# Optimization experiments

Hardware: AMD Instinct MI355X
Metric: run time of the kernel (lower is better)

Reference implementation:

```python
import jax, jax.numpy as jnp
import numpy as np
from jax import lax

BN_EPS = 1e-5


def _conv1d(h, w, b=None):
    # h: [B, Cin, L], w: [Cout, Cin, K], 'same' padding for odd K
    k = w.shape[-1]
    out = lax.conv_general_dilated(h, w, (1,), [(k // 2, k // 2)],
                                   dimension_numbers=('NCH', 'OIH', 'NCH'))
    if b is not None:
        out = out + b[None, :, None]
    return out


def _bn(h, gamma, beta):
    # eval-mode BatchNorm1d with running_mean=0, running_var=1
    return h * (gamma[None, :, None] / jnp.sqrt(1.0 + BN_EPS)) + beta[None, :, None]


def _encoder(h, cw, cb, rw, gammas, betas, aw, au):
    # h: [B, D, L] -> V: [B, C, F]
    t = jnp.tanh(_conv1d(h, cw, cb))
    t = _bn(t, gammas[0], betas[0])
    for i in range(rw.shape[0]):  # residual blocks
        t = jnp.tanh(_bn(_conv1d(t, rw[i]), gammas[i + 1], betas[i + 1]) + t)
    # label attention: w [A,F], u [C,A]
    Z = jnp.tanh(jnp.einsum('af,bfl->bal', aw, t))
    A = jax.nn.softmax(jnp.einsum('ca,bal->bcl', au, Z), axis=2)
    V = jnp.einsum('bfl,bcl->bcf', t, A)
    return V


def setup_inputs() -> dict:
    key = jax.random.key(0)
    ks = list(jax.random.split(key, 32))
    B, L, D, C, VOC, NE, N, E = 16, 4096, 256, 50, 50000, 20050, 512, 8192
    F, A, FFN = 100, 256, 128

    def rn(k, shape, s):
        return (jax.random.normal(k, shape, jnp.float32) * s).astype(jnp.float32)

    x = jax.random.randint(ks[0], (B, L), 0, VOC)
    attention_mask = jnp.ones((B, L), jnp.int32)
    nodes = jax.random.randint(ks[1], (B, N), 0, NE)
    src = jax.random.randint(ks[2], (B, E), 0, N)
    off = jax.random.randint(ks[3], (B, E), 1, N)
    dst = (src + off) % N  # guaranteed no self-loops
    edges = jnp.stack([src, dst], axis=1)  # [B, 2, E]

    inp = dict(x=x, attention_mask=attention_mask, nodes=nodes, edges=edges)
    inp['word_emb'] = rn(ks[4], (VOC, D), 0.02)
    inp['entity_emb'] = rn(ks[5], (NE, D), 0.02)
    i = 6
    for ksz in (3, 5, 9):
        inp[f'convw{ksz}'] = rn(ks[i], (F, D, ksz), (2.0 / (D * ksz)) ** 0.5); i += 1
        inp[f'convb{ksz}'] = jnp.zeros((F,), jnp.float32)
        inp[f'resw{ksz}'] = rn(ks[i], (2, F, F, ksz), (2.0 / (F * ksz)) ** 0.5); i += 1
    inp['bn_gamma'] = jnp.ones((3, 3, F), jnp.float32)
    inp['bn_beta'] = jnp.zeros((3, 3, F), jnp.float32)
    inp['attn_w'] = rn(ks[i], (3, A, F), 0.05); i += 1
    inp['attn_u'] = rn(ks[i], (3, C, A), 0.05); i += 1
    inp['gc1_w'] = rn(ks[i], (D, D), (1.0 / D) ** 0.5); i += 1
    inp['gc1_b'] = jnp.zeros((D,), jnp.float32)
    inp['gc2_w'] = rn(ks[i], (D, D), (1.0 / D) ** 0.5); i += 1
    inp['gc2_b'] = jnp.zeros((D,), jnp.float32)
    inp['fin1_w'] = rn(ks[i], (FFN, 3 * F + D), 0.05); i += 1
    inp['fin1_b'] = jnp.zeros((FFN,), jnp.float32)
    inp['fin2_w'] = rn(ks[i], (C, FFN), 0.05); i += 1
    inp['fin2_b'] = jnp.zeros((C,), jnp.float32)
    return inp


def reference(x, attention_mask, nodes, edges, word_emb, entity_emb,
              convw3, convb3, resw3, convw5, convb5, resw5, convw9, convb9, resw9,
              bn_gamma, bn_beta, attn_w, attn_u,
              gc1_w, gc1_b, gc2_w, gc2_b, fin1_w, fin1_b, fin2_w, fin2_b):
    C = fin2_b.shape[0]
    h = word_emb[x]                      # [B, L, D]
    h = jnp.transpose(h, (0, 2, 1))      # [B, D, L]

    Vs = []
    for i, (cw, cb, rw) in enumerate([(convw3, convb3, resw3),
                                      (convw5, convb5, resw5),
                                      (convw9, convb9, resw9)]):
        Vs.append(_encoder(h, cw, cb, rw, bn_gamma[i], bn_beta[i], attn_w[i], attn_u[i]))
    V = jnp.concatenate(Vs, axis=2)      # [B, C, 300]

    node_emb = entity_emb[nodes]         # [B, N, D]

    def per_graph(ne, ei):
        N = ne.shape[0]
        sl = jnp.arange(N)
        s = jnp.concatenate([ei[0], sl])  # GCNConv adds self-loops
        d = jnp.concatenate([ei[1], sl])
        deg = jax.ops.segment_sum(jnp.ones(s.shape[0], jnp.float32), d, num_segments=N)
        dinv = jnp.where(deg > 0, lax.rsqrt(deg), 0.0)
        norm = (dinv[s] * dinv[d])[:, None]

        def gconv(hh, W, b):
            return jax.ops.segment_sum((hh @ W.T)[s] * norm, d, num_segments=N) + b

        g = jax.nn.relu(gconv(ne, gc1_w, gc1_b))
        g = gconv(g, gc2_w, gc2_b)
        return g[:C]

    out_graphs = jax.vmap(per_graph)(node_emb, edges)  # [B, C, D]

    out = jnp.concatenate([out_graphs, V], axis=2)     # [B, C, D+300]
    hid = jax.nn.relu(jnp.einsum('bcf,hf->bch', out, fin1_w) + fin1_b)
    y_hat = jnp.sum(fin2_w[None] * hid, axis=2) + fin2_b  # [B, C]
    return y_hat
```

## Files before the change

kernel.cpp:

```cpp
#include <hip/hip_runtime.h>


#define CDIV(a,b) (((a)+(b)-1)/(b))

#define B_    16
#define L_    4096
#define D_    256
#define LP_   4112
#define POFF  8
#define F_    100
#define A_    256
#define C_    50
#define NN_   512
#define EE_   8192
#define ADJ_  8704
#define OC_   560

#define PLANE ((size_t)B_*LP_*128)
#define TTS   ((size_t)B_*128*L_)
#define SST   ((size_t)B_*64*L_)
#define VPS   ((size_t)B_*64*16*112)

#define WFC1_STRIDE ((size_t)9*8*8*512)
#define WFRES_STRIDE ((size_t)9*4*8*512)
#define WFAW_STRIDE ((size_t)4*16*512)
#define WFAU_STRIDE ((size_t)8*4*512)

typedef unsigned short u16;
using short8  = __attribute__((ext_vector_type(8))) short;
using short4v = __attribute__((ext_vector_type(4))) short;
using f32x4   = __attribute__((ext_vector_type(4))) float;

__device__ __forceinline__ u16 f2b(float f){
    unsigned u = __float_as_uint(f);
    u += 0x7FFF + ((u >> 16) & 1);
    return (u16)(u >> 16);
}
__device__ __forceinline__ float b2f(u16 h){ return __uint_as_float(((unsigned)h) << 16); }

__global__ void fill_i_k(int* p, int n, int v){
    int i = blockIdx.x*256 + threadIdx.x; if (i < n) p[i] = v;
}
__global__ void zero_pads3_k(u16* p){
    int idx = blockIdx.x*256 + threadIdx.x;
    if (idx >= 3*B_*16*128) return;
    int ch = idx & 127; int rest = idx >> 7;
    int pc = rest & 15; rest >>= 4;
    int b = rest & 15;  int br = rest >> 4;
    int col = (pc < 8) ? pc : (4096 + pc);
    p[(size_t)br*PLANE + ((size_t)b*LP_ + col)*128 + ch] = 0;
}

__global__ __launch_bounds__(256) void embed1_k(const int* __restrict__ x,
                                                const float* __restrict__ emb,
                                                u16* __restrict__ hH){
    int b = blockIdx.y;
    int col = blockIdx.x*8 + (threadIdx.x >> 5);
    int cg  = (threadIdx.x & 31) * 8;
    size_t o = ((size_t)b*LP_ + col)*D_ + cg;
    int l = col - POFF;
    short8 h0;
    if (l < 0 || l >= L_){
        #pragma unroll
        for (int i = 0; i < 8; ++i) h0[i] = 0;
    } else {
        int tok = x[b*L_ + l];
        const float* s = emb + (size_t)tok*D_ + cg;
        #pragma unroll
        for (int i = 0; i < 8; ++i) h0[i] = (short)f2b(s[i]);
    }
    *(short8*)(hH + o) = h0;
}

__device__ __forceinline__ void pack_frag(const float* src, u16* dst,
                                          int M, int K, int kt, int nch, int MTtot, int idx){
    int i = idx & 7, lane = (idx >> 3) & 63, rest = idx >> 9;
    int mt = rest % MTtot, r2 = rest / MTtot;
    int cc = r2 % nch,  j = r2 / nch;
    int m  = mt*16 + (lane & 15);
    int ch = cc*32 + (lane >> 4)*8 + i;
    float v = (m < M && ch < K) ? src[((size_t)m*K + ch)*kt + j] : 0.f;
    dst[(size_t)rest*512 + lane*8 + i] = f2b(v);
}
__global__ void pack_conv1_k(const float* w3, const float* w5, const float* w9, u16* dst){
    int br = blockIdx.y;
    int k = (br == 0) ? 3 : (br == 1) ? 5 : 9;
    const float* s = (br == 0) ? w3 : (br == 1) ? w5 : w9;
    int idx = blockIdx.x*256 + threadIdx.x;
    if (idx < k*8*8*512) pack_frag(s, dst + (size_t)br*WFC1_STRIDE, F_, 256, k, 8, 8, idx);
}
__global__ void pack_res_k(const float* w3, const float* w5, const float* w9, u16* dst){
    int br = blockIdx.y, blk = blockIdx.z;
    int k = (br == 0) ? 3 : (br == 1) ? 5 : 9;
    const float* s = ((br == 0) ? w3 : (br == 1) ? w5 : w9) + (size_t)blk*F_*F_*k;
    int idx = blockIdx.x*256 + threadIdx.x;
    if (idx < k*4*8*512) pack_frag(s, dst + (size_t)(br*2 + blk)*WFRES_STRIDE, F_, F_, k, 4, 8, idx);
}
__global__ void pack_aw_k(const float* aw, u16* dst){
    int br = blockIdx.y;
    int idx = blockIdx.x*256 + threadIdx.x;
    if (idx < 4*16*512) pack_frag(aw + (size_t)br*A_*F_, dst + (size_t)br*WFAW_STRIDE, A_, F_, 1, 4, 16, idx);
}
__global__ void pack_au_k(const float* au, u16* dst){
    int br = blockIdx.y;
    int idx = blockIdx.x*256 + threadIdx.x;
    if (idx < 8*4*512) pack_frag(au + (size_t)br*C_*A_, dst + (size_t)br*WFAU_STRIDE, C_, A_, 1, 8, 4, idx);
}
__global__ void transpose_fin1_k(const float* __restrict__ src, float* __restrict__ dst){
    int idx = blockIdx.x*256 + threadIdx.x;
    if (idx >= OC_*128) return;
    int h = idx & 127, j = idx >> 7;
    dst[idx] = (j < 556) ? src[h*556 + j] : 0.f;
}

template<int KT, int NCH>
__device__ __forceinline__ void conv_loop(
    const u16* __restrict__ inb, int CHp_in,
    const u16* __restrict__ wf,
    short* sm, int n0, int tid, int w, int lane, int q, int lr,
    f32x4 (&acc)[2][4])
{
    constexpr int NPASS = NCH / 4;
    for (int pass = 0; pass < NPASS; ++pass){
        #pragma unroll
        for (int s5 = 0; s5 < 5; ++s5){
            int idx = s5*256 + tid;
            int cc = idx / 320;
            int e = idx - cc*320;
            int col = e >> 2, qq = e & 3;
            *(short8*)(sm + cc*3200 + col*40 + qq*8) =
                *(const short8*)(inb + (size_t)(n0 + col)*CHp_in + (pass*4 + cc)*32 + qq*8);
        }
        __syncthreads();
        const u16* wbase = wf + ((size_t)(pass*4)*8 + w*2)*512 + lane*8;
        const short* bbase = sm + (8 - (KT >> 1) + lr)*40 + q*8;
        short8 Ac0 = *(const short8*)(wbase);
        short8 Ac1 = *(const short8*)(wbase + 512);
        #pragma unroll
        for (int it = 0; it < KT*4; ++it){
            const int j = it >> 2, cc = it & 3;
            short8 An0, An1;
            if (it + 1 < KT*4){
                const int jn = (it+1) >> 2, ccn = (it+1) & 3;
                const u16* fn = wbase + (size_t)(jn*NCH + ccn)*8*512;
                An0 = *(const short8*)(fn);
                An1 = *(const short8*)(fn + 512);
            }
            short8 Bv[4];
            #pragma unroll
            for (int n = 0; n < 4; ++n)
                Bv[n] = *(const short8*)(bbase + cc*3200 + (j + n*16)*40);
            #pragma unroll
            for (int n = 0; n < 4; ++n){
                acc[0][n] = __builtin_amdgcn_mfma_f32_16x16x32_bf16(Ac0, Bv[n], acc[0][n], 0,0,0);
                acc[1][n] = __builtin_amdgcn_mfma_f32_16x16x32_bf16(Ac1, Bv[n], acc[1][n], 0,0,0);
            }
            if (it + 1 < KT*4){ Ac0 = An0; Ac1 = An1; }
        }
        __syncthreads();
    }
}

template<int MODE, int NCH>
__global__ __launch_bounds__(256) void conv_mfma_k(
    const u16* __restrict__ in_base, int CHp_in, long in_bs,
    const u16* __restrict__ wf_base, long wf_bs,
    const float* __restrict__ bias0, const float* __restrict__ bias1,
    const float* __restrict__ bias2,
    const float* __restrict__ gamma_base, const float* __restrict__ beta_base, int layeroff,
    u16* __restrict__ out_base, u16* __restrict__ outT_base)
{
    __shared__ short sm[12800];
    const int tid = threadIdx.x, lane = tid & 63;
    const int w = tid >> 6;
    const int q = lane >> 4, lr = lane & 15;
    const int n0 = blockIdx.x * 64;
    const int b  = blockIdx.y;
    const int br = blockIdx.z;
    const u16* in = in_base + (size_t)br*in_bs;
    const u16* wf = wf_base + (size_t)br*wf_bs;
    const float* bias = (MODE == 0) ? ((br == 0) ? bias0 : (br == 1) ? bias1 : bias2) : nullptr;
    const float* gamma = gamma_base + br*300 + layeroff;
    const float* beta  = beta_base  + br*300 + layeroff;
    u16* out  = out_base + (size_t)br*PLANE;
    u16* outT = outT_base ? (outT_base + (size_t)br*TTS) : nullptr;
    const u16* inb = in + (size_t)b*LP_*CHp_in;

    f32x4 acc[2][4];
    #pragma unroll
    for (int t = 0; t < 2; ++t)
        #pragma unroll
        for (int n = 0; n < 4; ++n) acc[t][n] = (f32x4){0.f,0.f,0.f,0.f};

    if (br == 0)      conv_loop<3,NCH>(inb, CHp_in, wf, sm, n0, tid, w, lane, q, lr, acc);
    else if (br == 1) conv_loop<5,NCH>(inb, CHp_in, wf, sm, n0, tid, w, lane, q, lr, acc);
    else              conv_loop<9,NCH>(inb, CHp_in, wf, sm, n0, tid, w, lane, q, lr, acc);

    const float BNS = 0.9999950000374997f;
    for (int p = 0; p < 2; ++p){
        #pragma unroll
        for (int t = 0; t < 2; ++t){
            #pragma unroll
            for (int u = 0; u < 2; ++u){
                int n = p*2 + u;
                int mbase = w*32 + t*16 + q*4;
                int cl = u*16 + lr;
                int colg = n0 + n*16 + lr;
                float rsum[4] = {0.f,0.f,0.f,0.f};
                if (MODE == 1){
                    size_t ro = ((size_t)b*LP_ + POFF + colg)*CHp_in + mbase;
                    short4v rh = *(const short4v*)(in + ro);
                    #pragma unroll
                    for (int r = 0; r < 4; ++r) rsum[r] = b2f((u16)rh[r]);
                }
                short4v hv;
                #pragma unroll
                for (int r = 0; r < 4; ++r){
                    int mm = mbase + r;
                    float a = acc[t][n][r];
                    float v;
                    if (MODE == 0){
                        float bi=0.f, s=0.f, be=0.f;
                        if (mm < F_){ bi = bias[mm]; s = gamma[mm]*BNS; be = beta[mm]; }
                        v = tanhf(a + bi)*s + be;
                    } else {
                        float s=0.f, be=0.f;
                        if (mm < F_){ s = gamma[mm]*BNS; be = beta[mm]; }
                        v = tanhf(fmaf(a, s, be) + rsum[r]);
                    }
                    hv[r] = (short)f2b(v);
                }
                *(short4v*)(sm + cl*136 + mbase) = hv;
            }
        }
        __syncthreads();
        for (int idx = tid; idx < 512; idx += 256){
            int col = idx >> 4, q8 = idx & 15;
            short8 vv = *(const short8*)(sm + col*136 + q8*8);
            *(short8*)(out + ((size_t)b*LP_ + POFF + n0 + p*32 + col)*128 + q8*8) = vv;
        }
        if (outT){
            int f = tid & 127, half = tid >> 7;
            u16 vals[16];
            #pragma unroll
            for (int i = 0; i < 16; ++i) vals[i] = (u16)sm[(half*16 + i)*136 + f];
            short8 v0, v1;
            #pragma unroll
            for (int i = 0; i < 8; ++i){ v0[i] = (short)vals[i]; v1[i] = (short)vals[8+i]; }
            u16* dst = outT + ((size_t)b*128 + f)*L_ + n0 + p*32 + half*16;
            *(short8*)dst = v0;
            *(short8*)(dst + 8) = v1;
        }
        __syncthreads();
    }
}

__global__ __launch_bounds__(256) void attn_k(const u16* __restrict__ t_base,
                                              const u16* __restrict__ awf_base,
                                              const u16* __restrict__ auf_base,
                                              u16* __restrict__ S_base){
    __shared__ short sm[17408];
    const int tid = threadIdx.x, lane = tid & 63;
    const int w = tid >> 6, wm = w >> 1, wn = w & 1;
    const int q = lane >> 4, lr = lane & 15;
    const int n0 = blockIdx.x * 128;
    const int b  = blockIdx.y;
    const int br = blockIdx.z;
    const u16* tpl = t_base + (size_t)br*PLANE;
    const u16* awf = awf_base + (size_t)br*WFAW_STRIDE;
    const u16* auf = auf_base + (size_t)br*WFAU_STRIDE;
    u16* S = S_base + (size_t)br*SST;

    for (int idx = tid; idx < 2048; idx += 256){
        int col = idx >> 4, g = idx & 15;
        *(short8*)(sm + col*136 + g*8) =
            *(const short8*)(tpl + ((size_t)b*LP_ + POFF + n0 + col)*128 + g*8);
    }
    __syncthreads();

    f32x4 acc1[8][4];
    #pragma unroll
    for (int t = 0; t < 8; ++t)
        #pragma unroll
        for (int n = 0; n < 4; ++n) acc1[t][n] = (f32x4){0.f,0.f,0.f,0.f};
    for (int cc = 0; cc < 4; ++cc){
        short8 Af[8];
        const u16* fp = awf + (size_t)(cc*16 + wm*8)*512 + lane*8;
        #pragma unroll
        for (int t = 0; t < 8; ++t) Af[t] = *(const short8*)(fp + (size_t)t*512);
        short8 Bf[4];
        #pragma unroll
        for (int n = 0; n < 4; ++n)
            Bf[n] = *(const short8*)(sm + (wn*64 + n*16 + lr)*136 + cc*32 + q*8);
        #pragma unroll
        for (int t = 0; t < 8; ++t)
            #pragma unroll
            for (int n = 0; n < 4; ++n)
                acc1[t][n] = __builtin_amdgcn_mfma_f32_16x16x32_bf16(Af[t], Bf[n], acc1[t][n], 0,0,0);
    }
    __syncthreads();

    for (int p = 0; p < 2; ++p){
        if (wn == p){
            #pragma unroll
            for (int t = 0; t < 8; ++t){
                #pragma unroll
                for (int n = 0; n < 4; ++n){
                    int abase = wm*128 + t*16 + q*4;
                    int cl = n*16 + lr;
                    short4v zv;
                    #pragma unroll
                    for (int r = 0; r < 4; ++r) zv[r] = (short)f2b(tanhf(acc1[t][n][r]));
                    *(short4v*)(sm + cl*264 + abase) = zv;
                }
            }
        }
        __syncthreads();
        f32x4 acc2[4];
        #pragma unroll
        for (int t = 0; t < 4; ++t) acc2[t] = (f32x4){0.f,0.f,0.f,0.f};
        for (int cc = 0; cc < 8; ++cc){
            short8 Af2[4];
            const u16* fp2 = auf + (size_t)(cc*4)*512 + lane*8;
            #pragma unroll
            for (int t = 0; t < 4; ++t) Af2[t] = *(const short8*)(fp2 + (size_t)t*512);
            short8 Bf2 = *(const short8*)(sm + (w*16 + lr)*264 + cc*32 + q*8);
            #pragma unroll
            for (int t = 0; t < 4; ++t)
                acc2[t] = __builtin_amdgcn_mfma_f32_16x16x32_bf16(Af2[t], Bf2, acc2[t], 0,0,0);
        }
        #pragma unroll
        for (int t = 0; t < 4; ++t)
            #pragma unroll
            for (int r = 0; r < 4; ++r){
                int c = t*16 + q*4 + r;
                S[((size_t)b*64 + c)*L_ + n0 + p*64 + w*16 + lr] = f2b(acc2[t][r]);
            }
        __syncthreads();
    }
}

__global__ __launch_bounds__(256) void softmax_k(u16* __restrict__ S){
    int c = blockIdx.x, b = blockIdx.y, br = blockIdx.z, t = threadIdx.x;
    u16* p = S + (size_t)br*SST + ((size_t)b*64 + c)*L_;
    __shared__ float sh[256];
    float mx = -1e30f;
    for (int j = t; j < L_; j += 256) mx = fmaxf(mx, b2f(p[j]));
    sh[t] = mx; __syncthreads();
    for (int o = 128; o > 0; o >>= 1){ if (t < o) sh[t] = fmaxf(sh[t], sh[t+o]); __syncthreads(); }
    float m = sh[0]; __syncthreads();
    float sum = 0.f;
    for (int j = t; j < L_; j += 256){ float e = expf(b2f(p[j]) - m); p[j] = f2b(e); sum += e; }
    sh[t] = sum; __syncthreads();
    for (int o = 128; o > 0; o >>= 1){ if (t < o) sh[t] += sh[t+o]; __syncthreads(); }
    float inv = 1.0f / sh[0];
    for (int j = t; j < L_; j += 256) p[j] = f2b(b2f(p[j]) * inv);
}

__global__ __launch_bounds__(256) void v_mfma_k(const u16* __restrict__ tT_base,
                                                const u16* __restrict__ S_base,
                                                float* __restrict__ Vp_base){
    int cx = blockIdx.x, b = blockIdx.y, br = blockIdx.z;
    int w = threadIdx.x >> 6, lane = threadIdx.x & 63;
    int q = lane >> 4, lr = lane & 15;
    int l0 = cx*256;
    f32x4 acc[7];
    #pragma unroll
    for (int mt = 0; mt < 7; ++mt) acc[mt] = (f32x4){0.f,0.f,0.f,0.f};
    const u16* tb = tT_base + (size_t)br*TTS + (size_t)b*128*L_;
    const u16* Sb = S_base + (size_t)br*SST + ((size_t)b*64 + w*16 + lr)*L_;
    #pragma unroll
    for (int kk = 0; kk < 8; ++kk){
        int l = l0 + kk*32 + q*8;
        short8 Bf = *(const short8*)(Sb + l);
        #pragma unroll
        for (int mt = 0; mt < 7; ++mt){
            short8 Af = *(const short8*)(tb + (size_t)(mt*16 + lr)*L_ + l);
            acc[mt] = __builtin_amdgcn_mfma_f32_16x16x32_bf16(Af, Bf, acc[mt], 0,0,0);
        }
    }
    int c = w*16 + lr;
    if (c < C_){
        float* vp = Vp_base + (size_t)br*VPS + ((size_t)(b*64 + c)*16 + cx)*112;
        #pragma unroll
        for (int mt = 0; mt < 7; ++mt)
            *(f32x4*)(vp + mt*16 + q*4) = acc[mt];
    }
}

__global__ void reduce_v_k(const float* __restrict__ Vp, float* __restrict__ oc){
    int idx = blockIdx.x*256 + threadIdx.x;
    if (idx >= 3*B_*C_*F_) return;
    int f = idx % F_; int rest = idx / F_;
    int c = rest % C_; rest /= C_;
    int b = rest % B_; int br = rest / B_;
    const float* src = Vp + (size_t)br*VPS + ((size_t)(b*64 + c)*16)*112 + f;
    float s = 0.f;
    #pragma unroll
    for (int cx = 0; cx < 16; ++cx) s += src[cx*112];
    oc[((size_t)b*C_ + c)*OC_ + 256 + br*100 + f] = s;
}

__global__ void gather_nodes_k(const int* __restrict__ nodes, const float* __restrict__ emb,
                               float* __restrict__ ne){
    int idx = blockIdx.x*256 + threadIdx.x;
    if (idx >= B_*NN_*D_) return;
    int d = idx & 255, n = (idx >> 8) & 511, b = idx >> 17;
    ne[idx] = emb[(size_t)nodes[b*NN_ + n]*D_ + d];
}
__global__ void deg_count_k(const int* __restrict__ edges, int* __restrict__ deg){
    int idx = blockIdx.x*256 + threadIdx.x;
    if (idx >= B_*EE_) return;
    int b = idx >> 13, e = idx & (EE_-1);
    int dst = edges[b*2*EE_ + EE_ + e];
    atomicAdd(&deg[b*NN_ + dst], 1);
}
__global__ void dinv_k(const int* __restrict__ deg, float* __restrict__ dinv){
    int i = blockIdx.x*256 + threadIdx.x;
    if (i < B_*NN_) dinv[i] = 1.0f / sqrtf((float)deg[i]);
}
__global__ void scan_csr_k(const int* __restrict__ deg, int* __restrict__ rp, int* __restrict__ cur){
    int b = blockIdx.x, t = threadIdx.x;
    __shared__ int sh[NN_];
    int v = deg[b*NN_ + t];
    sh[t] = v; __syncthreads();
    for (int off = 1; off < NN_; off <<= 1){
        int x = (t >= off) ? sh[t-off] : 0;
        __syncthreads();
        sh[t] += x;
        __syncthreads();
    }
    int incl = sh[t], excl = incl - v;
    rp[b*513 + t] = excl;
    cur[b*NN_ + t] = excl;
    if (t == NN_-1) rp[b*513 + NN_] = incl;
}
__global__ void fill_csr_k(const int* __restrict__ edges, int* __restrict__ cur, int* __restrict__ adj){
    int e = blockIdx.x*256 + threadIdx.x, b = blockIdx.y;
    if (e >= ADJ_) return;
    int s, d;
    if (e < EE_){ s = edges[b*2*EE_ + e]; d = edges[b*2*EE_ + EE_ + e]; }
    else        { s = d = e - EE_; }
    int pos = atomicAdd(&cur[b*NN_ + d], 1);
    adj[b*ADJ_ + pos] = s;
}
__global__ __launch_bounds__(256) void gemm_nt_k(const float* __restrict__ A,
                                                 const float* __restrict__ W,
                                                 float* __restrict__ out){
    int b = blockIdx.z, n0 = blockIdx.x*64, i0 = blockIdx.y*64;
    __shared__ float aL[64][17], wL[64][17];
    int tid = threadIdx.x, tx = tid & 15, ty = tid >> 4;
    const float* Ab = A + (size_t)b*NN_*D_;
    float acc[4][4];
    #pragma unroll
    for (int r = 0; r < 4; ++r)
        #pragma unroll
        for (int i = 0; i < 4; ++i) acc[r][i] = 0.f;
    for (int j0 = 0; j0 < D_; j0 += 16){
        for (int idx = tid; idx < 1024; idx += 256){
            int r = idx >> 4, cc = idx & 15;
            aL[r][cc] = Ab[(size_t)(n0+r)*D_ + j0 + cc];
            wL[r][cc] = W[(size_t)(i0+r)*D_ + j0 + cc];
        }
        __syncthreads();
        #pragma unroll
        for (int kk = 0; kk < 16; ++kk){
            float av[4], wv[4];
            #pragma unroll
            for (int r = 0; r < 4; ++r) av[r] = aL[ty*4+r][kk];
            #pragma unroll
            for (int i = 0; i < 4; ++i) wv[i] = wL[tx*4+i][kk];
            #pragma unroll
            for (int r = 0; r < 4; ++r)
                #pragma unroll
                for (int i = 0; i < 4; ++i) acc[r][i] = fmaf(av[r], wv[i], acc[r][i]);
        }
        __syncthreads();
    }
    float* ob = out + (size_t)b*NN_*D_;
    #pragma unroll
    for (int r = 0; r < 4; ++r)
        #pragma unroll
        for (int i = 0; i < 4; ++i)
            ob[(size_t)(n0+ty*4+r)*D_ + i0+tx*4+i] = acc[r][i];
}
__global__ __launch_bounds__(256) void scatter_k(const float* __restrict__ xw,
                                                 const int* __restrict__ adj,
                                                 const int* __restrict__ rp,
                                                 const float* __restrict__ dinv,
                                                 const float* __restrict__ bias,
                                                 float* __restrict__ out,
                                                 int out_bs, int out_ld, int relu){
    int n = blockIdx.x, b = blockIdx.y, t = threadIdx.x;
    const int* rpb = rp + b*513;
    const int* adjb = adj + b*ADJ_;
    const float* xwb = xw + (size_t)b*NN_*D_;
    const float* dvb = dinv + b*NN_;
    int e0 = rpb[n], e1 = rpb[n+1];
    float acc = 0.f;
    for (int e = e0; e < e1; ++e){
        int s = adjb[e];
        acc = fmaf(xwb[(size_t)s*D_ + t], dvb[s], acc);
    }
    float v = fmaf(acc, dvb[n], bias[t]);
    if (relu) v = fmaxf(v, 0.f);
    out[(size_t)b*out_bs + (size_t)n*out_ld + t] = v;
}

__global__ __launch_bounds__(128) void final_k(const float* __restrict__ oc,
                                               const float* __restrict__ w1t,
                                               const float* __restrict__ b1,
                                               const float* __restrict__ w2,
                                               const float* __restrict__ b2,
                                               float* __restrict__ y){
    int c = blockIdx.x, b = blockIdx.y, h = threadIdx.x;
    __shared__ float row[OC_];
    __shared__ float red[128];
    const float* src = oc + ((size_t)b*C_ + c)*OC_;
    for (int j = h; j < OC_; j += 128) row[j] = src[j];
    __syncthreads();
    float acc = b1[h];
    #pragma unroll 8
    for (int j = 0; j < OC_; ++j) acc = fmaf(row[j], w1t[j*128 + h], acc);
    float hid = fmaxf(acc, 0.f);
    red[h] = hid * w2[c*128 + h];
    __syncthreads();
    for (int o = 64; o > 0; o >>= 1){ if (h < o) red[h] += red[h+o]; __syncthreads(); }
    if (h == 0) y[b*C_ + c] = red[0] + b2[c];
}

extern "C" void kernel_launch(void* const* d_in, const int* in_sizes, int n_in,
                              void* d_out, int out_size, void* d_ws, size_t ws_size,
                              hipStream_t stream){
    (void)in_sizes; (void)n_in; (void)out_size; (void)ws_size;
    const int*   x          = (const int*)d_in[0];
    const int*   nodes      = (const int*)d_in[2];
    const int*   edges      = (const int*)d_in[3];
    const float* word_emb   = (const float*)d_in[4];
    const float* entity_emb = (const float*)d_in[5];
    const float* bn_gamma   = (const float*)d_in[15];
    const float* bn_beta    = (const float*)d_in[16];
    const float* gc1_w      = (const float*)d_in[19];
    const float* gc1_b      = (const float*)d_in[20];
    const float* gc2_w      = (const float*)d_in[21];
    const float* gc2_b      = (const float*)d_in[22];
    const float* fin1_w     = (const float*)d_in[23];
    const float* fin1_b     = (const float*)d_in[24];
    const float* fin2_w     = (const float*)d_in[25];
    const float* fin2_b     = (const float*)d_in[26];
    float* y = (float*)d_out;

    char* base = (char*)d_ws;
    size_t off = 0;
    auto alloc = [&](size_t bytes) -> char* {
        char* p = base + off;
        off += ((bytes + 255) / 256) * 256;
        return p;
    };
    u16* t0 = (u16*)alloc(3*PLANE*2);
    u16* t1 = (u16*)alloc(3*PLANE*2);
    u16* hH = t1;
    u16* tT = (u16*)alloc(3*TTS*2);
    u16* S  = (u16*)alloc(3*SST*2);
    char* G = alloc((size_t)3*B_*NN_*D_*4);
    float* ne = (float*)G;
    float* xw = ne + (size_t)B_*NN_*D_;
    float* g1 = xw + (size_t)B_*NN_*D_;
    float* Vpart = (float*)G;
    float* ocat = (float*)alloc((size_t)B_*C_*OC_*4);
    u16* wfc1  = (u16*)alloc(3*WFC1_STRIDE*2);
    u16* wfres = (u16*)alloc(6*WFRES_STRIDE*2);
    u16* wfaw  = (u16*)alloc(3*WFAW_STRIDE*2);
    u16* wfau  = (u16*)alloc(3*WFAU_STRIDE*2);
    float* w1t   = (float*)alloc((size_t)OC_*128*4);
    float* dinvp = (float*)alloc((size_t)B_*NN_*4);
    int* deg = (int*)alloc((size_t)B_*NN_*4);
    int* rpB = (int*)alloc((size_t)B_*513*4);
    int* cur = (int*)alloc((size_t)B_*NN_*4);
    int* adj = (int*)alloc((size_t)B_*ADJ_*4);

    fill_i_k<<<CDIV(B_*NN_,256),256,0,stream>>>(deg, B_*NN_, 1);
    zero_pads3_k<<<CDIV(3*B_*16*128,256),256,0,stream>>>(t0);
    pack_conv1_k<<<dim3(CDIV(9*8*8*512,256),3),256,0,stream>>>(
        (const float*)d_in[6], (const float*)d_in[9], (const float*)d_in[12], wfc1);
    pack_res_k<<<dim3(CDIV(9*4*8*512,256),3,2),256,0,stream>>>(
        (const float*)d_in[8], (const float*)d_in[11], (const float*)d_in[14], wfres);
    pack_aw_k<<<dim3(CDIV(4*16*512,256),3),256,0,stream>>>((const float*)d_in[17], wfaw);
    pack_au_k<<<dim3(CDIV(8*4*512,256),3),256,0,stream>>>((const float*)d_in[18], wfau);

    embed1_k<<<dim3(LP_/8, B_),256,0,stream>>>(x, word_emb, hH);

    gather_nodes_k<<<CDIV(B_*NN_*D_,256),256,0,stream>>>(nodes, entity_emb, ne);
    deg_count_k<<<CDIV(B_*EE_,256),256,0,stream>>>(edges, deg);
    dinv_k<<<CDIV(B_*NN_,256),256,0,stream>>>(deg, dinvp);
    scan_csr_k<<<B_,NN_,0,stream>>>(deg, rpB, cur);
    fill_csr_k<<<dim3(CDIV(ADJ_,256),B_),256,0,stream>>>(edges, cur, adj);
    gemm_nt_k<<<dim3(NN_/64, D_/64, B_),256,0,stream>>>(ne, gc1_w, xw);
    scatter_k<<<dim3(NN_,B_),256,0,stream>>>(xw, adj, rpB, dinvp, gc1_b, g1, NN_*D_, D_, 1);
    gemm_nt_k<<<dim3(NN_/64, D_/64, B_),256,0,stream>>>(g1, gc2_w, xw);
    scatter_k<<<dim3(C_,B_),256,0,stream>>>(xw, adj, rpB, dinvp, gc2_b, ocat, C_*OC_, OC_, 0);

    dim3 gc(64, B_, 3), ga(32, B_, 3);
    conv_mfma_k<0,8><<<gc,256,0,stream>>>(hH, 256, 0,
        wfc1, (long)WFC1_STRIDE,
        (const float*)d_in[7], (const float*)d_in[10], (const float*)d_in[13],
        bn_gamma, bn_beta, 0, t0, nullptr);
    zero_pads3_k<<<CDIV(3*B_*16*128,256),256,0,stream>>>(t1);
    conv_mfma_k<1,4><<<gc,256,0,stream>>>(t0, 128, (long)PLANE,
        wfres, (long)(2*WFRES_STRIDE),
        nullptr, nullptr, nullptr,
        bn_gamma, bn_beta, 100, t1, nullptr);
    conv_mfma_k<1,4><<<gc,256,0,stream>>>(t1, 128, (long)PLANE,
        wfres + WFRES_STRIDE, (long)(2*WFRES_STRIDE),
        nullptr, nullptr, nullptr,
        bn_gamma, bn_beta, 200, t0, tT);
    attn_k<<<ga,256,0,stream>>>(t0, wfaw, wfau, S);
    softmax_k<<<dim3(C_,B_,3),256,0,stream>>>(S);
    v_mfma_k<<<dim3(16,B_,3),256,0,stream>>>(tT, S, Vpart);
    reduce_v_k<<<CDIV(3*B_*C_*F_,256),256,0,stream>>>(Vpart, ocat);

    transpose_fin1_k<<<CDIV(OC_*128,256),256,0,stream>>>(fin1_w, w1t);
    final_k<<<dim3(C_,B_),128,0,stream>>>(ocat, w1t, fin1_b, fin2_w, fin2_b, y);
}
```

Before: 687.7 us.

## Retile conv warps to 2x2 layout and shrink attention block tile to 64 columns

The conv kernel's warp tiling changes from each warp owning 32 output channels across all 64 columns to a 2x2 layout, where each warp owns 64 channels by 32 columns. This loads four weight fragments and two LDS B fragments per step instead of two and four, cutting LDS reads while adding register pressure. The attention kernel's tile drops from 128 to 64 columns per block, with a launch grid twice as large. That removes the two-phase loop and halves its accumulators, which should raise occupancy and parallelism at the cost of reloading weight fragments more often.

```diff
diff --git a/kernel.cpp b/kernel.cpp
--- a/kernel.cpp
+++ b/kernel.cpp
@@ -117,8 +117,8 @@
 __device__ __forceinline__ void conv_loop(
     const u16* __restrict__ inb, int CHp_in,
     const u16* __restrict__ wf,
-    short* sm, int n0, int tid, int w, int lane, int q, int lr,
-    f32x4 (&acc)[2][4])
+    short* sm, int n0, int tid, int wm, int wn, int lane, int q, int lr,
+    f32x4 (&acc)[4][2])
 {
     constexpr int NPASS = NCH / 4;
     for (int pass = 0; pass < NPASS; ++pass){
@@ -132,30 +132,33 @@
                 *(const short8*)(inb + (size_t)(n0 + col)*CHp_in + (pass*4 + cc)*32 + qq*8);
         }
         __syncthreads();
-        const u16* wbase = wf + ((size_t)(pass*4)*8 + w*2)*512 + lane*8;
-        const short* bbase = sm + (8 - (KT >> 1) + lr)*40 + q*8;
-        short8 Ac0 = *(const short8*)(wbase);
-        short8 Ac1 = *(const short8*)(wbase + 512);
+        const u16* wbase = wf + ((size_t)(pass*4)*8 + wm*4)*512 + lane*8;
+        const short* bbase = sm + (8 - (KT >> 1) + wn*32 + lr)*40 + q*8;
+        short8 Ac[4], An[4];
+        #pragma unroll
+        for (int t = 0; t < 4; ++t) Ac[t] = *(const short8*)(wbase + (size_t)t*512);
         #pragma unroll
         for (int it = 0; it < KT*4; ++it){
             const int j = it >> 2, cc = it & 3;
-            short8 An0, An1;
             if (it + 1 < KT*4){
                 const int jn = (it+1) >> 2, ccn = (it+1) & 3;
                 const u16* fn = wbase + (size_t)(jn*NCH + ccn)*8*512;
-                An0 = *(const short8*)(fn);
-                An1 = *(const short8*)(fn + 512);
+                #pragma unroll
+                for (int t = 0; t < 4; ++t) An[t] = *(const short8*)(fn + (size_t)t*512);
             }
-            short8 Bv[4];
-            #pragma unroll
-            for (int n = 0; n < 4; ++n)
+            short8 Bv[2];
+            #pragma unroll
+            for (int n = 0; n < 2; ++n)
                 Bv[n] = *(const short8*)(bbase + cc*3200 + (j + n*16)*40);
             #pragma unroll
-            for (int n = 0; n < 4; ++n){
-                acc[0][n] = __builtin_amdgcn_mfma_f32_16x16x32_bf16(Ac0, Bv[n], acc[0][n], 0,0,0);
-                acc[1][n] = __builtin_amdgcn_mfma_f32_16x16x32_bf16(Ac1, Bv[n], acc[1][n], 0,0,0);
+            for (int t = 0; t < 4; ++t)
+                #pragma unroll
+                for (int n = 0; n < 2; ++n)
+                    acc[t][n] = __builtin_amdgcn_mfma_f32_16x16x32_bf16(Ac[t], Bv[n], acc[t][n], 0,0,0);
+            if (it + 1 < KT*4){
+                #pragma unroll
+                for (int t = 0; t < 4; ++t) Ac[t] = An[t];
             }
-            if (it + 1 < KT*4){ Ac0 = An0; Ac1 = An1; }
         }
         __syncthreads();
     }
@@ -172,7 +175,7 @@
 {
     __shared__ short sm[12800];
     const int tid = threadIdx.x, lane = tid & 63;
-    const int w = tid >> 6;
+    const int w = tid >> 6, wm = w >> 1, wn = w & 1;
     const int q = lane >> 4, lr = lane & 15;
     const int n0 = blockIdx.x * 64;
     const int b  = blockIdx.y;
@@ -186,51 +189,52 @@
     u16* outT = outT_base ? (outT_base + (size_t)br*TTS) : nullptr;
     const u16* inb = in + (size_t)b*LP_*CHp_in;
 
-    f32x4 acc[2][4];
-    #pragma unroll
-    for (int t = 0; t < 2; ++t)
-        #pragma unroll
-        for (int n = 0; n < 4; ++n) acc[t][n] = (f32x4){0.f,0.f,0.f,0.f};
-
-    if (br == 0)      conv_loop<3,NCH>(inb, CHp_in, wf, sm, n0, tid, w, lane, q, lr, acc);
-    else if (br == 1) conv_loop<5,NCH>(inb, CHp_in, wf, sm, n0, tid, w, lane, q, lr, acc);
-    else              conv_loop<9,NCH>(inb, CHp_in, wf, sm, n0, tid, w, lane, q, lr, acc);
+    f32x4 acc[4][2];
+    #pragma unroll
+    for (int t = 0; t < 4; ++t)
+        #pragma unroll
+        for (int n = 0; n < 2; ++n) acc[t][n] = (f32x4){0.f,0.f,0.f,0.f};
+
+    if (br == 0)      conv_loop<3,NCH>(inb, CHp_in, wf, sm, n0, tid, wm, wn, lane, q, lr, acc);
+    else if (br == 1) conv_loop<5,NCH>(inb, CHp_in, wf, sm, n0, tid, wm, wn, lane, q, lr, acc);
+    else              conv_loop<9,NCH>(inb, CHp_in, wf, sm, n0, tid, wm, wn, lane, q, lr, acc);
 
     const float BNS = 0.9999950000374997f;
     for (int p = 0; p < 2; ++p){
-        #pragma unroll
-        for (int t = 0; t < 2; ++t){
-            #pragma unroll
-            for (int u = 0; u < 2; ++u){
-                int n = p*2 + u;
-                int mbase = w*32 + t*16 + q*4;
-                int cl = u*16 + lr;
-                int colg = n0 + n*16 + lr;
-                float rsum[4] = {0.f,0.f,0.f,0.f};
-                if (MODE == 1){
-                    size_t ro = ((size_t)b*LP_ + POFF + colg)*CHp_in + mbase;
-                    short4v rh = *(const short4v*)(in + ro);
+        if (wn == p){
+            #pragma unroll
+            for (int t = 0; t < 4; ++t){
+                #pragma unroll
+                for (int n = 0; n < 2; ++n){
+                    int mbase = wm*64 + t*16 + q*4;
+                    int cl = n*16 + lr;
+                    int colg = n0 + p*32 + cl;
+                    float rsum[4] = {0.f,0.f,0.f,0.f};
+                    if (MODE == 1){
+                        size_t ro = ((size_t)b*LP_ + POFF + colg)*CHp_in + mbase;
+                        short4v rh = *(const short4v*)(in + ro);
+                        #pragma unroll
+                        for (int r = 0; r < 4; ++r) rsum[r] = b2f((u16)rh[r]);
+                    }
+                    short4v hv;
                     #pragma unroll
-                    for (int r = 0; r < 4; ++r) rsum[r] = b2f((u16)rh[r]);
+                    for (int r = 0; r < 4; ++r){
+                        int mm = mbase + r;
+                        float a = acc[t][n][r];
+                        float v;
+                        if (MODE == 0){
+                            float bi=0.f, s=0.f, be=0.f;
+                            if (mm < F_){ bi = bias[mm]; s = gamma[mm]*BNS; be = beta[mm]; }
+                            v = tanhf(a + bi)*s + be;
+                        } else {
+                            float s=0.f, be=0.f;
+                            if (mm < F_){ s = gamma[mm]*BNS; be = beta[mm]; }
+                            v = tanhf(fmaf(a, s, be) + rsum[r]);
+                        }
+                        hv[r] = (short)f2b(v);
+                    }
+                    *(short4v*)(sm + cl*136 + mbase) = hv;
                 }
-                short4v hv;
-                #pragma unroll
-                for (int r = 0; r < 4; ++r){
-                    int mm = mbase + r;
-                    float a = acc[t][n][r];
-                    float v;
-                    if (MODE == 0){
-                        float bi=0.f, s=0.f, be=0.f;
-                        if (mm < F_){ bi = bias[mm]; s = gamma[mm]*BNS; be = beta[mm]; }
-                        v = tanhf(a + bi)*s + be;
-                    } else {
-                        float s=0.f, be=0.f;
-                        if (mm < F_){ s = gamma[mm]*BNS; be = beta[mm]; }
-                        v = tanhf(fmaf(a, s, be) + rsum[r]);
-                    }
-                    hv[r] = (short)f2b(v);
-                }
-                *(short4v*)(sm + cl*136 + mbase) = hv;
             }
         }
         __syncthreads();
@@ -259,11 +263,11 @@
                                               const u16* __restrict__ awf_base,
                                               const u16* __restrict__ auf_base,
                                               u16* __restrict__ S_base){
-    __shared__ short sm[17408];
+    __shared__ short sm[16896];
     const int tid = threadIdx.x, lane = tid & 63;
-    const int w = tid >> 6, wm = w >> 1, wn = w & 1;
+    const int w = tid >> 6;
     const int q = lane >> 4, lr = lane & 15;
-    const int n0 = blockIdx.x * 128;
+    const int n0 = blockIdx.x * 64;
     const int b  = blockIdx.y;
     const int br = blockIdx.z;
     const u16* tpl = t_base + (size_t)br*PLANE;
@@ -271,73 +275,69 @@
     const u16* auf = auf_base + (size_t)br*WFAU_STRIDE;
     u16* S = S_base + (size_t)br*SST;
 
-    for (int idx = tid; idx < 2048; idx += 256){
+    for (int idx = tid; idx < 1024; idx += 256){
         int col = idx >> 4, g = idx & 15;
         *(short8*)(sm + col*136 + g*8) =
             *(const short8*)(tpl + ((size_t)b*LP_ + POFF + n0 + col)*128 + g*8);
     }
     __syncthreads();
 
-    f32x4 acc1[8][4];
-    #pragma unroll
-    for (int t = 0; t < 8; ++t)
+    f32x4 acc1[4][4];
+    #pragma unroll
+    for (int t = 0; t < 4; ++t)
         #pragma unroll
         for (int n = 0; n < 4; ++n) acc1[t][n] = (f32x4){0.f,0.f,0.f,0.f};
     for (int cc = 0; cc < 4; ++cc){
-        short8 Af[8];
-        const u16* fp = awf + (size_t)(cc*16 + wm*8)*512 + lane*8;
-        #pragma unroll
-        for (int t = 0; t < 8; ++t) Af[t] = *(const short8*)(fp + (size_t)t*512);
+        short8 Af[4];
+        const u16* fp = awf + (size_t)(cc*16 + w*4)*512 + lane*8;
+        #pragma unroll
+        for (int t = 0; t < 4; ++t) Af[t] = *(const short8*)(fp + (size_t)t*512);
         short8 Bf[4];
         #pragma unroll
         for (int n = 0; n < 4; ++n)
-            Bf[n] = *(const short8*)(sm + (wn*64 + n*16 + lr)*136 + cc*32 + q*8);
-        #pragma unroll
-        for (int t = 0; t < 8; ++t)
+            Bf[n] = *(const short8*)(sm + (n*16 + lr)*136 + cc*32 + q*8);
+        #pragma unroll
+        for (int t = 0; t < 4; ++t)
             #pragma unroll
             for (int n = 0; n < 4; ++n)
                 acc1[t][n] = __builtin_amdgcn_mfma_f32_16x16x32_bf16(Af[t], Bf[n], acc1[t][n], 0,0,0);
     }
     __syncthreads();
 
-    for (int p = 0; p < 2; ++p){
-        if (wn == p){
-            #pragma unroll
-            for (int t = 0; t < 8; ++t){
-                #pragma unroll
-                for (int n = 0; n < 4; ++n){
-                    int abase = wm*128 + t*16 + q*4;
-                    int cl = n*16 + lr;
-                    short4v zv;
-                    #pragma unroll
-                    for (int r = 0; r < 4; ++r) zv[r] = (short)f2b(tanhf(acc1[t][n][r]));
-                    *(short4v*)(sm + cl*264 + abase) = zv;
-                }
-            }
-        }
-        __syncthreads();
-        f32x4 acc2[4];
-        #pragma unroll
-        for (int t = 0; t < 4; ++t) acc2[t] = (f32x4){0.f,0.f,0.f,0.f};
-        for (int cc = 0; cc < 8; ++cc){
-            short8 Af2[4];
-            const u16* fp2 = auf + (size_t)(cc*4)*512 + lane*8;
-            #pragma unroll
-            for (int t = 0; t < 4; ++t) Af2[t] = *(const short8*)(fp2 + (size_t)t*512);
-            short8 Bf2 = *(const short8*)(sm + (w*16 + lr)*264 + cc*32 + q*8);
-            #pragma unroll
-            for (int t = 0; t < 4; ++t)
-                acc2[t] = __builtin_amdgcn_mfma_f32_16x16x32_bf16(Af2[t], Bf2, acc2[t], 0,0,0);
-        }
+    #pragma unroll
+    for (int t = 0; t < 4; ++t){
+        #pragma unroll
+        for (int n = 0; n < 4; ++n){
+            int abase = w*64 + t*16 + q*4;
+            int cl = n*16 + lr;
+            short4v zv;
+            #pragma unroll
+            for (int r = 0; r < 4; ++r) zv[r] = (short)f2b(tanhf(acc1[t][n][r]));
+            *(short4v*)(sm + cl*264 + abase) = zv;
+        }
+    }
+    __syncthreads();
+
+    f32x4 acc2[4];
+    #pragma unroll
+    for (int t = 0; t < 4; ++t) acc2[t] = (f32x4){0.f,0.f,0.f,0.f};
+    for (int cc = 0; cc < 8; ++cc){
+        short8 Af2[4];
+        const u16* fp2 = auf + (size_t)(cc*4)*512 + lane*8;
+        #pragma unroll
+        for (int t = 0; t < 4; ++t) Af2[t] = *(const short8*)(fp2 + (size_t)t*512);
+        short8 Bf2 = *(const short8*)(sm + (w*16 + lr)*264 + cc*32 + q*8);
         #pragma unroll
         for (int t = 0; t < 4; ++t)
-            #pragma unroll
-            for (int r = 0; r < 4; ++r){
-                int c = t*16 + q*4 + r;
-                S[((size_t)b*64 + c)*L_ + n0 + p*64 + w*16 + lr] = f2b(acc2[t][r]);
-            }
-        __syncthreads();
-    }
+            acc2[t] = __builtin_amdgcn_mfma_f32_16x16x32_bf16(Af2[t], Bf2, acc2[t], 0,0,0);
+    }
+    #pragma unroll
+    for (int t = 0; t < 4; ++t)
+        #pragma unroll
+        for (int r = 0; r < 4; ++r){
+            int c = t*16 + q*4 + r;
+            S[((size_t)b*64 + c)*L_ + n0 + w*16 + lr] = f2b(acc2[t][r]);
+        }
 }
 
 __global__ __launch_bounds__(256) void softmax_k(u16* __restrict__ S){
@@ -600,7 +600,7 @@
     gemm_nt_k<<<dim3(NN_/64, D_/64, B_),256,0,stream>>>(g1, gc2_w, xw);
     scatter_k<<<dim3(C_,B_),256,0,stream>>>(xw, adj, rpB, dinvp, gc2_b, ocat, C_*OC_, OC_, 0);
 
-    dim3 gc(64, B_, 3), ga(32, B_, 3);
+    dim3 gc(64, B_, 3), ga(64, B_, 3);
     conv_mfma_k<0,8><<<gc,256,0,stream>>>(hH, 256, 0,
         wfc1, (long)WFC1_STRIDE,
         (const float*)d_in[7], (const float*)d_in[10], (const float*)d_in[13],
```

Result: slower. 798.5 us (+16.1%).
